# Kernel tuning notes

Hardware: AMD Instinct MI355X
Metric: run time of the kernel (lower is better)

## Reference

```python
import jax, jax.numpy as jnp
import numpy as np

N_EMBED = 1024
EMBED_DIM = 64
BETA = 0.25


def setup_inputs() -> dict:
    key = jax.random.key(0)
    k1, k2 = jax.random.split(key)
    z = jax.random.normal(k1, (16, EMBED_DIM, 64, 64), dtype=jnp.float32)
    # torch init: uniform(-1/n_embed, 1/n_embed)
    embed_weight = jax.random.uniform(
        k2, (N_EMBED, EMBED_DIM), dtype=jnp.float32,
        minval=-1.0 / N_EMBED, maxval=1.0 / N_EMBED)
    return {"z": z, "embed_weight": embed_weight}


def reference(z, embed_weight):
    # z: (B, C, H, W) with C == embed_dim
    n_embed = embed_weight.shape[0]
    zp = jnp.transpose(z, (0, 2, 3, 1))                     # (B,H,W,C)
    zf = zp.reshape(-1, zp.shape[-1])                       # (N,C)
    # squared euclidean distances: ||z||^2 - 2 z.e + ||e||^2
    dist = (jnp.sum(zf * zf, axis=1, keepdims=True)
            - 2.0 * (zf @ embed_weight.T)
            + jnp.sum(embed_weight * embed_weight, axis=1))  # (N,n_embed)
    embed_index = jnp.argmin(dist, axis=1)                  # (N,)
    embed_onehot = jax.nn.one_hot(embed_index, n_embed, dtype=zf.dtype)
    # one-hot @ codebook is just a gather
    quantize = embed_weight[embed_index].reshape(zp.shape)  # (B,H,W,C)
    vq_loss = (jnp.mean((jax.lax.stop_gradient(quantize) - zp) ** 2)
               + BETA * jnp.mean((quantize - jax.lax.stop_gradient(zp)) ** 2))
    # straight-through estimator
    quantize_st = zp + jax.lax.stop_gradient(quantize - zp)
    e_mean = jnp.mean(embed_onehot, axis=0)
    perplexity = jnp.exp(-jnp.sum(e_mean * jnp.log(e_mean + 1e-10)))
    quantize_out = jnp.transpose(quantize_st, (0, 3, 1, 2))  # (B,C,H,W)
    return (quantize_out, vq_loss, perplexity, embed_onehot, embed_index)
```

## Files before the change

### kernel.cpp

```cpp
#include <hip/hip_runtime.h>
#include <math.h>


#define HW 4096
#define OUT_Q    0ull
#define OUT_LOSS 4194304ull
#define OUT_PERP 4194305ull
#define OUT_OH   4194306ull
#define OUT_IDX  71303170ull
#define CHUNK 256
#define NCHUNK 4

__global__ void vq_setup(const float* __restrict__ W,
                         float* __restrict__ wsf, int* __restrict__ wsi) {
    const int b = blockIdx.x, tid = threadIdx.x;
    if (tid < 64) wsi[b * 64 + tid] = 0;
    if (b == 0 && tid == 0) wsf[1024] = 0.0f;
    const int wave = tid >> 6, lane = tid & 63;
    for (int p = 0; p < 16; ++p) {
        const int code = b * 64 + p * 4 + wave;
        const float a = W[code * 64 + lane];
        const float sq = __fmul_rn(a, a);
        float t = sq;
        #pragma unroll
        for (int m = 1; m < 8; ++m) t = __fadd_rn(t, __shfl(sq, lane + 8 * m, 64));
        const float u  = __fadd_rn(t, __shfl_xor(t, 1, 64));
        const float v  = __fadd_rn(u, __shfl_xor(u, 2, 64));
        const float w2 = __fadd_rn(v, __shfl_xor(v, 4, 64));
        if (lane == 0) wsf[1028 + code] = w2;
    }
}

__global__ __launch_bounds__(256, 2)
void vq_main(const float* __restrict__ Z, const float* __restrict__ W,
             float* __restrict__ out, float* __restrict__ wsf, int* __restrict__ wsi) {
    __shared__ __align__(16) float smem[17984];
    float* ldsW   = smem;
    float* ldsC   = smem + 16384;
    float* cand_v = smem + 17408;
    int*   cand_i = (int*)(smem + 17664);
    int*   mi     = (int*)(smem + 17920);

    const int tid  = threadIdx.x;
    const int wave = tid >> 6;
    const int lane = tid & 63;
    const int blk  = blockIdx.x;
    const int b    = blk >> 6;
    const int hw0  = (blk & 63) << 6;
    const int rowbase = b * HW + hw0;

    {
        const float4* gs = (const float4*)W;
        float4* ls = (float4*)ldsW;
        #pragma unroll
        for (int i = 0; i < 16; ++i) ls[i * 256 + tid] = gs[i * 256 + tid];
    }
    ((float4*)ldsC)[tid] = ((const float4*)(wsf + 1028))[tid];

    const float* zb = Z + (size_t)b * 64 * HW + hw0 + lane;
    float zr[64];
    #pragma unroll
    for (int c = 0; c < 64; ++c) zr[c] = zb[(size_t)c * HW];

    float r[8];
    #pragma unroll
    for (int j = 0; j < 8; ++j) r[j] = __fmul_rn(zr[j], zr[j]);
    #pragma unroll
    for (int i = 8; i < 64; i += 8) {
        #pragma unroll
        for (int j = 0; j < 8; ++j) r[j] = __fadd_rn(r[j], __fmul_rn(zr[i + j], zr[i + j]));
    }
    const float A = __fadd_rn(__fadd_rn(__fadd_rn(r[0], r[1]), __fadd_rn(r[2], r[3])),
                              __fadd_rn(__fadd_rn(r[4], r[5]), __fadd_rn(r[6], r[7])));

    float bestv = __builtin_huge_valf();
    int   besti = 0;

    for (int ch = 0; ch < NCHUNK; ++ch) {
        __syncthreads();
        #pragma unroll 2
        for (int cc = 0; cc < 64; ++cc) {
            const int cl = cc * 4 + wave;
            const float* wrow = ldsW + cl * 64;
            float dot = 0.0f;
            #pragma unroll
            for (int k4 = 0; k4 < 16; ++k4) {
                const float4 wv = *(const float4*)(wrow + k4 * 4);
                dot = __fmaf_rn(zr[4 * k4 + 0], wv.x, dot);
                dot = __fmaf_rn(zr[4 * k4 + 1], wv.y, dot);
                dot = __fmaf_rn(zr[4 * k4 + 2], wv.z, dot);
                dot = __fmaf_rn(zr[4 * k4 + 3], wv.w, dot);
            }
            const int code = ch * CHUNK + cl;
            const float d = __fadd_rn(__fsub_rn(A, 2.0f * dot), ldsC[code]);
            if (d < bestv) { bestv = d; besti = code; }
        }
        if (ch + 1 < NCHUNK) {
            __syncthreads();
            const float4* gs = (const float4*)(W + (size_t)(ch + 1) * CHUNK * 64);
            float4* ls = (float4*)ldsW;
            #pragma unroll
            for (int i = 0; i < 16; ++i) ls[i * 256 + tid] = gs[i * 256 + tid];
        }
    }

    cand_v[wave * 64 + lane] = bestv;
    cand_i[wave * 64 + lane] = besti;
    __syncthreads();
    if (wave == 0) {
        float bv = cand_v[lane]; int bi = cand_i[lane];
        #pragma unroll
        for (int s = 1; s < 4; ++s) {
            const float v  = cand_v[s * 64 + lane];
            const int   i2 = cand_i[s * 64 + lane];
            if (v < bv || (v == bv && i2 < bi)) { bv = v; bi = i2; }
        }
        mi[lane] = bi;
        out[OUT_IDX + rowbase + lane] = (float)bi;
        atomicAdd(&wsi[bi], 1);
    }
    __syncthreads();

    float* qT = smem;
    {
        const int m = mi[lane];
        const float4* wq = (const float4*)(W + m * 64);
        #pragma unroll
        for (int j4 = 0; j4 < 4; ++j4) {
            const float4 q = wq[wave * 4 + j4];
            const int c0 = wave * 16 + j4 * 4;
            qT[lane * 65 + c0 + 0] = q.x;
            qT[lane * 65 + c0 + 1] = q.y;
            qT[lane * 65 + c0 + 2] = q.z;
            qT[lane * 65 + c0 + 3] = q.w;
        }
    }
    __syncthreads();

    float lsum = 0.0f;
    #pragma unroll
    for (int j = 0; j < 16; ++j) {
        const int c = j * 4 + wave;
        const float qv = qT[lane * 65 + c];
        const float zv = zr[c];
        const float dd = __fsub_rn(qv, zv);
        lsum = __fmaf_rn(dd, dd, lsum);
        out[OUT_Q + (size_t)(b * 64 + c) * HW + hw0 + lane] = __fadd_rn(zv, dd);
    }
    #pragma unroll
    for (int s = 32; s > 0; s >>= 1) lsum += __shfl_xor(lsum, s, 64);
    if (lane == 0) atomicAdd(wsf + 1024, lsum);

    for (int i = 0; i < 64; ++i) {
        const int m = mi[i];
        float* basep = out + OUT_OH + (size_t)(rowbase + i) * 1024;
        const int c0 = tid * 2;
        float2 v0, v1;
        v0.x = (c0       == m) ? 1.0f : 0.0f;
        v0.y = (c0 + 1   == m) ? 1.0f : 0.0f;
        v1.x = (c0 + 512 == m) ? 1.0f : 0.0f;
        v1.y = (c0 + 513 == m) ? 1.0f : 0.0f;
        *(float2*)(basep + c0)       = v0;
        *(float2*)(basep + 512 + c0) = v1;
    }
}

__global__ void vq_final(const int* __restrict__ wsi, const float* __restrict__ wsf,
                         float* __restrict__ out) {
    __shared__ double red[256];
    const int tid = threadIdx.x;
    double s = 0.0;
    for (int j = tid; j < 1024; j += 256) {
        const float e  = (float)wsi[j] * (1.0f / 65536.0f);
        const float lg = logf(__fadd_rn(e, 1e-10f));
        s += (double)__fmul_rn(e, lg);
    }
    red[tid] = s;
    __syncthreads();
    for (int st = 128; st > 0; st >>= 1) {
        if (tid < st) red[tid] += red[tid + st];
        __syncthreads();
    }
    if (tid == 0) {
        out[OUT_PERP] = expf((float)(-red[0]));
        const float ms = wsf[1024] * (1.0f / 4194304.0f);
        out[OUT_LOSS] = __fadd_rn(ms, __fmul_rn(0.25f, ms));
    }
}

extern "C" void kernel_launch(void* const* d_in, const int* in_sizes, int n_in,
                              void* d_out, int out_size, void* d_ws, size_t ws_size,
                              hipStream_t stream) {
    const float* Z = (const float*)d_in[0];
    const float* W = (const float*)d_in[1];
    float* out = (float*)d_out;
    float* wsf = (float*)d_ws;
    int*   wsi = (int*)d_ws;
    vq_setup<<<16,   256, 0, stream>>>(W, wsf, wsi);
    vq_main <<<1024, 256, 0, stream>>>(Z, W, out, wsf, wsi);
    vq_final<<<1,    256, 0, stream>>>(wsi, wsf, out);
}
```

Baseline: 482.9 us.

## Stream codebook rows through scalar loads instead of LDS staging

Measured after the change: 461.5 us. 4.4% less time.

```diff
diff --git a/kernel.cpp b/kernel.cpp
--- a/kernel.cpp
+++ b/kernel.cpp
@@ -8,8 +8,8 @@
 #define OUT_PERP 4194305ull
 #define OUT_OH   4194306ull
 #define OUT_IDX  71303170ull
-#define CHUNK 256
-#define NCHUNK 4
+
+typedef float f32x16 __attribute__((ext_vector_type(16)));
 
 __global__ void vq_setup(const float* __restrict__ W,
                          float* __restrict__ wsf, int* __restrict__ wsi) {
@@ -31,15 +31,14 @@
     }
 }
 
-__global__ __launch_bounds__(256, 2)
+__global__ __launch_bounds__(256, 4)
 void vq_main(const float* __restrict__ Z, const float* __restrict__ W,
              float* __restrict__ out, float* __restrict__ wsf, int* __restrict__ wsi) {
-    __shared__ __align__(16) float smem[17984];
-    float* ldsW   = smem;
-    float* ldsC   = smem + 16384;
-    float* cand_v = smem + 17408;
-    int*   cand_i = (int*)(smem + 17664);
-    int*   mi     = (int*)(smem + 17920);
+    __shared__ __align__(16) float qT[64 * 65];
+    __shared__ __align__(16) float ldsC[1024];
+    __shared__ float cand_v[256];
+    __shared__ int   cand_i[256];
+    __shared__ int   mi[64];
 
     const int tid  = threadIdx.x;
     const int wave = tid >> 6;
@@ -49,12 +48,6 @@
     const int hw0  = (blk & 63) << 6;
     const int rowbase = b * HW + hw0;
 
-    {
-        const float4* gs = (const float4*)W;
-        float4* ls = (float4*)ldsW;
-        #pragma unroll
-        for (int i = 0; i < 16; ++i) ls[i * 256 + tid] = gs[i * 256 + tid];
-    }
     ((float4*)ldsC)[tid] = ((const float4*)(wsf + 1028))[tid];
 
     const float* zb = Z + (size_t)b * 64 * HW + hw0 + lane;
@@ -73,35 +66,37 @@
     const float A = __fadd_rn(__fadd_rn(__fadd_rn(r[0], r[1]), __fadd_rn(r[2], r[3])),
                               __fadd_rn(__fadd_rn(r[4], r[5]), __fadd_rn(r[6], r[7])));
 
+    __syncthreads();
+
+    const float* Wwave = (const float*)((const char*)W +
+                         __builtin_amdgcn_readfirstlane(wave << 8));
+
     float bestv = __builtin_huge_valf();
     int   besti = 0;
 
-    for (int ch = 0; ch < NCHUNK; ++ch) {
-        __syncthreads();
-        #pragma unroll 2
-        for (int cc = 0; cc < 64; ++cc) {
-            const int cl = cc * 4 + wave;
-            const float* wrow = ldsW + cl * 64;
-            float dot = 0.0f;
-            #pragma unroll
-            for (int k4 = 0; k4 < 16; ++k4) {
-                const float4 wv = *(const float4*)(wrow + k4 * 4);
-                dot = __fmaf_rn(zr[4 * k4 + 0], wv.x, dot);
-                dot = __fmaf_rn(zr[4 * k4 + 1], wv.y, dot);
-                dot = __fmaf_rn(zr[4 * k4 + 2], wv.z, dot);
-                dot = __fmaf_rn(zr[4 * k4 + 3], wv.w, dot);
-            }
-            const int code = ch * CHUNK + cl;
-            const float d = __fadd_rn(__fsub_rn(A, 2.0f * dot), ldsC[code]);
-            if (d < bestv) { bestv = d; besti = code; }
-        }
-        if (ch + 1 < NCHUNK) {
-            __syncthreads();
-            const float4* gs = (const float4*)(W + (size_t)(ch + 1) * CHUNK * 64);
-            float4* ls = (float4*)ldsW;
-            #pragma unroll
-            for (int i = 0; i < 16; ++i) ls[i * 256 + tid] = gs[i * 256 + tid];
-        }
+    for (int i = 0; i < 256; ++i) {
+        const int code = i * 4 + wave;
+        const float* wrow = (const float*)((const char*)Wwave + (i << 10));
+        f32x16 a0, a1, a2, a3;
+        asm volatile(
+            "s_load_dwordx16 %0, %4, 0x0\n\t"
+            "s_load_dwordx16 %1, %4, 0x40\n\t"
+            "s_load_dwordx16 %2, %4, 0x80\n\t"
+            "s_load_dwordx16 %3, %4, 0xc0\n\t"
+            "s_waitcnt lgkmcnt(0)"
+            : "=&s"(a0), "=&s"(a1), "=&s"(a2), "=&s"(a3)
+            : "s"(wrow));
+        float dot = 0.0f;
+        #pragma unroll
+        for (int k = 0; k < 16; ++k) dot = __fmaf_rn(zr[k],      a0[k], dot);
+        #pragma unroll
+        for (int k = 0; k < 16; ++k) dot = __fmaf_rn(zr[16 + k], a1[k], dot);
+        #pragma unroll
+        for (int k = 0; k < 16; ++k) dot = __fmaf_rn(zr[32 + k], a2[k], dot);
+        #pragma unroll
+        for (int k = 0; k < 16; ++k) dot = __fmaf_rn(zr[48 + k], a3[k], dot);
+        const float d = __fadd_rn(__fsub_rn(A, 2.0f * dot), ldsC[code]);
+        if (d < bestv) { bestv = d; besti = code; }
     }
 
     cand_v[wave * 64 + lane] = bestv;
@@ -121,7 +116,6 @@
     }
     __syncthreads();
 
-    float* qT = smem;
     {
         const int m = mi[lane];
         const float4* wq = (const float4*)(W + m * 64);
```
